# Optimization experiments

Measured on AMD Instinct MI355X. Metric: run time of the kernel, lower is better.

The kernel has to match this reference:

```python
import jax, jax.numpy as jnp
import numpy as np

N_NODES = 50000
N_EDGES = 600000
D = 128  # in_channels == out_channels
LN_EPS = 1e-5


def _mlp(h, W1, b1, W2, b2, ln_g, ln_b):
    # anemoi MLP: Linear -> SiLU -> Linear -> LayerNorm
    h = jax.nn.silu(h @ W1 + b1)
    h = h @ W2 + b2
    mu = jnp.mean(h, axis=-1, keepdims=True)
    var = jnp.var(h, axis=-1, keepdims=True)
    return (h - mu) * jax.lax.rsqrt(var + LN_EPS) * ln_g + ln_b


def setup_inputs() -> dict:
    key = jax.random.key(0)
    ks = jax.random.split(key, 12)
    s = lambda fan_in: 1.0 / np.sqrt(fan_in)
    inp = {
        "x": jax.random.normal(ks[0], (N_NODES, D), dtype=jnp.float32),
        "edge_attr": jax.random.normal(ks[1], (N_EDGES, D), dtype=jnp.float32),
        "edge_index": jax.random.randint(ks[2], (2, N_EDGES), 0, N_NODES, dtype=jnp.int32),
        # conv edge-MLP params: in = 3*D (x_dst, x_src, edge_attr)
        "eW1": jax.random.uniform(ks[3], (3 * D, D), jnp.float32, -s(3 * D), s(3 * D)),
        "eb1": jnp.zeros((D,), jnp.float32),
        "eW2": jax.random.uniform(ks[4], (D, D), jnp.float32, -s(D), s(D)),
        "eb2": jnp.zeros((D,), jnp.float32),
        "eln_g": jnp.ones((D,), jnp.float32),
        "eln_b": jnp.zeros((D,), jnp.float32),
        # node MLP params: in = 2*D (x, aggregated messages)
        "nW1": jax.random.uniform(ks[5], (2 * D, D), jnp.float32, -s(2 * D), s(2 * D)),
        "nb1": jnp.zeros((D,), jnp.float32),
        "nW2": jax.random.uniform(ks[6], (D, D), jnp.float32, -s(D), s(D)),
        "nb2": jnp.zeros((D,), jnp.float32),
        "nln_g": jnp.ones((D,), jnp.float32),
        "nln_b": jnp.zeros((D,), jnp.float32),
    }
    return inp


def reference(x, edge_attr, edge_index,
              eW1, eb1, eW2, eb2, eln_g, eln_b,
              nW1, nb1, nW2, nb2, nln_g, nln_b):
    src = edge_index[0]  # j
    dst = edge_index[1]  # i
    # GraphConv.message: edge MLP over cat([x_i, x_j, edge_attr])
    edge_in = jnp.concatenate([x[dst], x[src], edge_attr], axis=1)  # [E, 3D]
    edges_new = _mlp(edge_in, eW1, eb1, eW2, eb2, eln_g, eln_b)      # [E, D]
    # aggregate: scatter-add to destination nodes (chunking sums to the same result)
    out = jax.ops.segment_sum(edges_new, dst, num_segments=x.shape[0])  # [N, D]
    # node update: concat + MLP + residual
    nodes_new = _mlp(jnp.concatenate([x, out], axis=1), nW1, nb1, nW2, nb2, nln_g, nln_b) + x
    return nodes_new, edges_new
```

## Files before the change

kernel.cpp:

```cpp
#include <hip/hip_runtime.h>

#define D       128
#define NNODES  50000
#define NEDGES  600000
#define TE      64
#define TN      64
#define BLK     256
#define LN_EPS  1e-5f

typedef float  fx4    __attribute__((ext_vector_type(4)));
typedef float  f32x4  __attribute__((ext_vector_type(4)));
typedef __bf16 bf16x4 __attribute__((ext_vector_type(4)));
typedef __bf16 bf16x8 __attribute__((ext_vector_type(8)));

#define EW1F_OFF 0
#define EW2F_OFF (128 * 384)
#define NW1F_OFF (EW2F_OFF + 128 * 128)
#define NW2F_OFF (NW1F_OFF + 128 * 256)
#define WS_ELEMS (NW2F_OFF + 128 * 128)
#define W_BYTES  (WS_ELEMS * 2)
#define PD_OFF      ((size_t)W_BYTES)
#define PS_OFF      (PD_OFF + (size_t)NNODES * D * 4)
#define WS_NEED_PRE (PS_OFF + (size_t)NNODES * D * 4)

__device__ __forceinline__ float silu_f(float z) {
    return z * (1.0f / (1.0f + __expf(-z)));
}

__global__ __launch_bounds__(256) void prep_weights(
    const float* __restrict__ eW1, const float* __restrict__ eW2,
    const float* __restrict__ nW1, const float* __restrict__ nW2,
    __bf16* __restrict__ ws)
{
    int idx = blockIdx.x * 256 + threadIdx.x;
    if (idx >= WS_ELEMS) return;
    const float* src;
    int local;
    if (idx < EW2F_OFF)      { src = eW1; local = idx; }
    else if (idx < NW1F_OFF) { src = eW2; local = idx - EW2F_OFF; }
    else if (idx < NW2F_OFF) { src = nW1; local = idx - NW1F_OFF; }
    else                     { src = nW2; local = idx - NW2F_OFF; }
    const int f   = local >> 9;
    const int rem = local & 511;
    const int l   = rem >> 3;
    const int j   = rem & 7;
    const int ks  = f >> 3;
    const int nf  = f & 7;
    const int n   = (nf << 4) + (l & 15);
    const int k   = (ks << 5) + ((l >> 4) << 3) + j;
    ws[idx] = (__bf16)src[(size_t)k * D + n];
}

__global__ __launch_bounds__(256) void pre_nodes(
    const float* __restrict__ x,
    const __bf16* __restrict__ W1f,
    const float* __restrict__ b1,
    float* __restrict__ Pd,
    float* __restrict__ Ps)
{
    __shared__ __bf16 xt[TN][136];

    const int tid = threadIdx.x;
    const int r0g = blockIdx.x * TN;
    const int lane  = tid & 63;
    const int wid   = tid >> 6;
    const int wrow0 = wid << 4;
    const int c16   = lane & 15;
    const int kq    = lane >> 4;
    const int ks8   = kq << 3;
    const int lo8   = lane << 3;

    #pragma unroll
    for (int pass = 0; pass < 8; ++pass) {
        const int row = wrow0 + (pass << 1) + (lane >> 5);
        const int gr  = r0g + row;
        const int c4  = (lane & 31) << 2;
        fx4 v = {0.f, 0.f, 0.f, 0.f};
        if (gr < NNODES) v = *(const fx4*)&x[(size_t)gr * D + c4];
        bf16x4 h;
        #pragma unroll
        for (int j = 0; j < 4; ++j) h[j] = (__bf16)v[j];
        *(bf16x4*)&xt[row][c4] = h;
    }

    f32x4 acc_d[8], acc_s[8];
    #pragma unroll
    for (int nf = 0; nf < 8; ++nf) {
        acc_d[nf] = (f32x4){0.f, 0.f, 0.f, 0.f};
        acc_s[nf] = (f32x4){0.f, 0.f, 0.f, 0.f};
    }

    #pragma unroll
    for (int ks = 0; ks < 4; ++ks) {
        bf16x8 a = *(const bf16x8*)&xt[wrow0 + c16][(ks << 5) + ks8];
        const __bf16* wpd = W1f + ((size_t)(ks << 3) << 9) + lo8;
        const __bf16* wps = W1f + ((size_t)((4 + ks) << 3) << 9) + lo8;
        #pragma unroll
        for (int nf = 0; nf < 8; ++nf) {
            bf16x8 bd = *(const bf16x8*)(wpd + (nf << 9));
            bf16x8 bs = *(const bf16x8*)(wps + (nf << 9));
            acc_d[nf] = __builtin_amdgcn_mfma_f32_16x16x32_bf16(a, bd, acc_d[nf], 0, 0, 0);
            acc_s[nf] = __builtin_amdgcn_mfma_f32_16x16x32_bf16(a, bs, acc_s[nf], 0, 0, 0);
        }
    }

    #pragma unroll
    for (int nf = 0; nf < 8; ++nf) {
        const int col = nf * 16 + c16;
        const float bb = b1[col];
        #pragma unroll
        for (int r = 0; r < 4; ++r) {
            const int row = r0g + wrow0 + kq * 4 + r;
            if (row < NNODES) {
                Pd[(size_t)row * D + col] = acc_d[nf][r] + bb;
                Ps[(size_t)row * D + col] = acc_s[nf][r];
            }
        }
    }
}

__global__ __launch_bounds__(BLK, 5) void edge_kernel_pre(
    const float* __restrict__ edge_attr,
    const int*   __restrict__ edge_index,
    const float* __restrict__ Pd,
    const float* __restrict__ Ps,
    const __bf16* __restrict__ W1f,
    const __bf16* __restrict__ W2f,
    const float* __restrict__ b2,
    const float* __restrict__ lng, const float* __restrict__ lnb,
    float* __restrict__ edges_out,
    float* __restrict__ agg)
{
    __shared__ __bf16 sum_t[TE][136];

    const int tid = threadIdx.x;
    const int e0g = blockIdx.x * TE;
    const int lane  = tid & 63;
    const int wid   = tid >> 6;
    const int wrow0 = wid << 4;
    const int c16   = lane & 15;
    const int kq    = lane >> 4;
    const int ks8   = kq << 3;
    const int lo8   = lane << 3;

    #pragma unroll
    for (int pass = 0; pass < 8; ++pass) {
        const int row = wrow0 + (pass << 1) + (lane >> 5);
        const int ge  = e0g + row;
        const int dn  = edge_index[NEDGES + ge];
        const int sn  = edge_index[ge];
        const int c4  = (lane & 31) << 2;
        fx4 a = *(const fx4*)&Pd[(size_t)dn * D + c4];
        fx4 b = *(const fx4*)&Ps[(size_t)sn * D + c4];
        bf16x4 h;
        #pragma unroll
        for (int j = 0; j < 4; ++j) h[j] = (__bf16)(a[j] + b[j]);
        *(bf16x4*)&sum_t[row][c4] = h;
    }

    bf16x8 aE[4];
    {
        const float* ep = edge_attr + (size_t)(e0g + wrow0 + c16) * D + ks8;
        #pragma unroll
        for (int ks2 = 0; ks2 < 4; ++ks2) {
            fx4 v0 = *(const fx4*)(ep + (ks2 << 5));
            fx4 v1 = *(const fx4*)(ep + (ks2 << 5) + 4);
            bf16x8 a;
            #pragma unroll
            for (int j = 0; j < 4; ++j) { a[j] = (__bf16)v0[j]; a[j + 4] = (__bf16)v1[j]; }
            aE[ks2] = a;
        }
    }

    f32x4 acc[8];
    #pragma unroll
    for (int nf = 0; nf < 8; ++nf) acc[nf] = (f32x4){0.f, 0.f, 0.f, 0.f};

    #pragma unroll
    for (int ks2 = 0; ks2 < 4; ++ks2) {
        const __bf16* wp = W1f + ((size_t)((8 + ks2) << 3) << 9) + lo8;
        #pragma unroll
        for (int nf = 0; nf < 8; ++nf) {
            bf16x8 b = *(const bf16x8*)(wp + (nf << 9));
            acc[nf] = __builtin_amdgcn_mfma_f32_16x16x32_bf16(aE[ks2], b, acc[nf], 0, 0, 0);
        }
    }

    #pragma unroll
    for (int nf = 0; nf < 8; ++nf) {
        #pragma unroll
        for (int r = 0; r < 4; ++r) {
            const int row = wrow0 + kq * 4 + r;
            const int col = nf * 16 + c16;
            float z = acc[nf][r] + (float)sum_t[row][col];
            sum_t[row][col] = (__bf16)silu_f(z);
        }
    }

    f32x4 acc2[8];
    #pragma unroll
    for (int nf = 0; nf < 8; ++nf) acc2[nf] = (f32x4){0.f, 0.f, 0.f, 0.f};

    #pragma unroll
    for (int ks = 0; ks < 4; ++ks) {
        bf16x8 a = *(const bf16x8*)&sum_t[wrow0 + c16][(ks << 5) + ks8];
        const __bf16* wp = W2f + ((size_t)(ks << 3) << 9) + lo8;
        #pragma unroll
        for (int nf = 0; nf < 8; ++nf) {
            bf16x8 b = *(const bf16x8*)(wp + (nf << 9));
            acc2[nf] = __builtin_amdgcn_mfma_f32_16x16x32_bf16(a, b, acc2[nf], 0, 0, 0);
        }
    }

    float b2v[8], gv[8], bvv[8];
    #pragma unroll
    for (int nf = 0; nf < 8; ++nf) {
        b2v[nf] = b2[nf * 16 + c16];
        gv[nf]  = lng[nf * 16 + c16];
        bvv[nf] = lnb[nf * 16 + c16];
    }

    float s[4] = {0.f, 0.f, 0.f, 0.f}, q[4] = {0.f, 0.f, 0.f, 0.f};
    #pragma unroll
    for (int nf = 0; nf < 8; ++nf)
        #pragma unroll
        for (int r = 0; r < 4; ++r) {
            float zz = acc2[nf][r] + b2v[nf];
            acc2[nf][r] = zz;
            s[r] += zz;
            q[r] += zz * zz;
        }
    #pragma unroll
    for (int m = 1; m <= 8; m <<= 1)
        #pragma unroll
        for (int r = 0; r < 4; ++r) {
            s[r] += __shfl_xor(s[r], m, 64);
            q[r] += __shfl_xor(q[r], m, 64);
        }

    #pragma unroll
    for (int r = 0; r < 4; ++r) {
        const float mu   = s[r] * (1.0f / 128.0f);
        const float var  = q[r] * (1.0f / 128.0f) - mu * mu;
        const float rstd = rsqrtf(var + LN_EPS);
        const int row = wrow0 + kq * 4 + r;
        const int ge  = e0g + row;
        const int dn  = edge_index[NEDGES + ge];
        const size_t erow = (size_t)ge * D;
        float* ap = agg + (size_t)dn * D;
        #pragma unroll
        for (int nf = 0; nf < 8; ++nf) {
            const int col = nf * 16 + c16;
            float o = (acc2[nf][r] - mu) * rstd * gv[nf] + bvv[nf];
            edges_out[erow + col] = o;
            atomicAdd(ap + col, o);
        }
    }
}

__global__ __launch_bounds__(BLK, 4) void edge_kernel_fb(
    const float* __restrict__ x,
    const float* __restrict__ edge_attr,
    const int*   __restrict__ edge_index,
    const __bf16* __restrict__ W1f,
    const float* __restrict__ b1,
    const __bf16* __restrict__ W2f,
    const float* __restrict__ b2,
    const float* __restrict__ lng, const float* __restrict__ lnb,
    float* __restrict__ edges_out,
    float* __restrict__ agg)
{
    __shared__ __bf16 in_t[TE][264];
    __shared__ int    src_s[TE], dst_s[TE];

    const int tid = threadIdx.x;
    const int e0g = blockIdx.x * TE;

    if (tid < TE) {
        src_s[tid] = edge_index[e0g + tid];
        dst_s[tid] = edge_index[NEDGES + e0g + tid];
    }
    __syncthreads();

    const int lane  = tid & 63;
    const int wid   = tid >> 6;
    const int wrow0 = wid << 4;
    const int c16   = lane & 15;
    const int kq    = lane >> 4;
    const int ks8   = kq << 3;
    const int lo8   = lane << 3;

    bf16x8 aE[4];
    {
        const float* ep = edge_attr + (size_t)(e0g + wrow0 + c16) * D + ks8;
        #pragma unroll
        for (int ks2 = 0; ks2 < 4; ++ks2) {
            fx4 v0 = *(const fx4*)(ep + (ks2 << 5));
            fx4 v1 = *(const fx4*)(ep + (ks2 << 5) + 4);
            bf16x8 a;
            #pragma unroll
            for (int j = 0; j < 4; ++j) { a[j] = (__bf16)v0[j]; a[j + 4] = (__bf16)v1[j]; }
            aE[ks2] = a;
        }
    }

    #pragma unroll
    for (int it = 0; it < 8; ++it) {
        const int idx = tid + it * BLK;
        const int e   = idx >> 5;
        const int c4  = (idx & 31) << 2;
        fx4 v = *(const fx4*)&x[(size_t)dst_s[e] * D + c4];
        bf16x4 h;
        #pragma unroll
        for (int j = 0; j < 4; ++j) h[j] = (__bf16)v[j];
        *(bf16x4*)&in_t[e][c4] = h;
    }
    #pragma unroll
    for (int it = 0; it < 8; ++it) {
        const int idx = tid + it * BLK;
        const int e   = idx >> 5;
        const int c4  = (idx & 31) << 2;
        fx4 v = *(const fx4*)&x[(size_t)src_s[e] * D + c4];
        bf16x4 h;
        #pragma unroll
        for (int j = 0; j < 4; ++j) h[j] = (__bf16)v[j];
        *(bf16x4*)&in_t[e][128 + c4] = h;
    }
    __syncthreads();

    f32x4 acc[8];
    #pragma unroll
    for (int nf = 0; nf < 8; ++nf) acc[nf] = (f32x4){0.f, 0.f, 0.f, 0.f};

    #pragma unroll
    for (int ks = 0; ks < 12; ++ks) {
        bf16x8 a = (ks < 8) ? *(const bf16x8*)&in_t[wrow0 + c16][(ks << 5) + ks8]
                            : aE[ks - 8];
        const __bf16* wp = W1f + ((size_t)(ks << 3) << 9) + lo8;
        #pragma unroll
        for (int nf = 0; nf < 8; ++nf) {
            bf16x8 b = *(const bf16x8*)(wp + (nf << 9));
            acc[nf] = __builtin_amdgcn_mfma_f32_16x16x32_bf16(a, b, acc[nf], 0, 0, 0);
        }
    }

    #pragma unroll
    for (int nf = 0; nf < 8; ++nf) {
        const float bb = b1[nf * 16 + c16];
        #pragma unroll
        for (int r = 0; r < 4; ++r) {
            float h = silu_f(acc[nf][r] + bb);
            in_t[wrow0 + kq * 4 + r][nf * 16 + c16] = (__bf16)h;
        }
    }

    f32x4 acc2[8];
    #pragma unroll
    for (int nf = 0; nf < 8; ++nf) acc2[nf] = (f32x4){0.f, 0.f, 0.f, 0.f};

    #pragma unroll
    for (int ks = 0; ks < 4; ++ks) {
        bf16x8 a = *(const bf16x8*)&in_t[wrow0 + c16][(ks << 5) + ks8];
        const __bf16* wp = W2f + ((size_t)(ks << 3) << 9) + lo8;
        #pragma unroll
        for (int nf = 0; nf < 8; ++nf) {
            bf16x8 b = *(const bf16x8*)(wp + (nf << 9));
            acc2[nf] = __builtin_amdgcn_mfma_f32_16x16x32_bf16(a, b, acc2[nf], 0, 0, 0);
        }
    }

    float b2v[8], gv[8], bvv[8];
    #pragma unroll
    for (int nf = 0; nf < 8; ++nf) {
        b2v[nf] = b2[nf * 16 + c16];
        gv[nf]  = lng[nf * 16 + c16];
        bvv[nf] = lnb[nf * 16 + c16];
    }

    float s[4] = {0.f, 0.f, 0.f, 0.f}, q[4] = {0.f, 0.f, 0.f, 0.f};
    #pragma unroll
    for (int nf = 0; nf < 8; ++nf)
        #pragma unroll
        for (int r = 0; r < 4; ++r) {
            float zz = acc2[nf][r] + b2v[nf];
            acc2[nf][r] = zz;
            s[r] += zz;
            q[r] += zz * zz;
        }
    #pragma unroll
    for (int m = 1; m <= 8; m <<= 1)
        #pragma unroll
        for (int r = 0; r < 4; ++r) {
            s[r] += __shfl_xor(s[r], m, 64);
            q[r] += __shfl_xor(q[r], m, 64);
        }

    #pragma unroll
    for (int r = 0; r < 4; ++r) {
        const float mu   = s[r] * (1.0f / 128.0f);
        const float var  = q[r] * (1.0f / 128.0f) - mu * mu;
        const float rstd = rsqrtf(var + LN_EPS);
        const int row = wrow0 + kq * 4 + r;
        const size_t erow = (size_t)(e0g + row) * D;
        float* ap = agg + (size_t)dst_s[row] * D;
        #pragma unroll
        for (int nf = 0; nf < 8; ++nf) {
            const int col = nf * 16 + c16;
            float o = (acc2[nf][r] - mu) * rstd * gv[nf] + bvv[nf];
            edges_out[erow + col] = o;
            atomicAdd(ap + col, o);
        }
    }
}

__global__ __launch_bounds__(BLK, 4) void node_kernel(
    const float* __restrict__ x,
    const float* __restrict__ agg,
    const __bf16* __restrict__ W1f,
    const float* __restrict__ b1,
    const __bf16* __restrict__ W2f,
    const float* __restrict__ b2,
    const float* __restrict__ lng, const float* __restrict__ lnb,
    float* __restrict__ nodes_out)
{
    __shared__ __bf16 in_t[TN][264];

    const int tid = threadIdx.x;
    const int r0g = blockIdx.x * TN;

    #pragma unroll
    for (int it = 0; it < 8; ++it) {
        const int idx = tid + it * BLK;
        const int e   = idx >> 5;
        const int c4  = (idx & 31) << 2;
        const int row = r0g + e;
        fx4 v = {0.f, 0.f, 0.f, 0.f};
        if (row < NNODES) v = *(const fx4*)&x[(size_t)row * D + c4];
        bf16x4 h;
        #pragma unroll
        for (int j = 0; j < 4; ++j) h[j] = (__bf16)v[j];
        *(bf16x4*)&in_t[e][c4] = h;
    }
    #pragma unroll
    for (int it = 0; it < 8; ++it) {
        const int idx = tid + it * BLK;
        const int e   = idx >> 5;
        const int c4  = (idx & 31) << 2;
        const int row = r0g + e;
        fx4 v = {0.f, 0.f, 0.f, 0.f};
        if (row < NNODES) v = *(const fx4*)&agg[(size_t)row * D + c4];
        bf16x4 h;
        #pragma unroll
        for (int j = 0; j < 4; ++j) h[j] = (__bf16)v[j];
        *(bf16x4*)&in_t[e][128 + c4] = h;
    }
    __syncthreads();

    const int lane  = tid & 63;
    const int wid   = tid >> 6;
    const int wrow0 = wid << 4;
    const int c16   = lane & 15;
    const int kq    = lane >> 4;
    const int ks8   = kq << 3;
    const int lo8   = lane << 3;

    f32x4 acc[8];
    #pragma unroll
    for (int nf = 0; nf < 8; ++nf) acc[nf] = (f32x4){0.f, 0.f, 0.f, 0.f};

    #pragma unroll
    for (int ks = 0; ks < 8; ++ks) {
        bf16x8 a = *(const bf16x8*)&in_t[wrow0 + c16][(ks << 5) + ks8];
        const __bf16* wp = W1f + ((size_t)(ks << 3) << 9) + lo8;
        #pragma unroll
        for (int nf = 0; nf < 8; ++nf) {
            bf16x8 b = *(const bf16x8*)(wp + (nf << 9));
            acc[nf] = __builtin_amdgcn_mfma_f32_16x16x32_bf16(a, b, acc[nf], 0, 0, 0);
        }
    }

    #pragma unroll
    for (int nf = 0; nf < 8; ++nf) {
        const float bb = b1[nf * 16 + c16];
        #pragma unroll
        for (int r = 0; r < 4; ++r) {
            float h = silu_f(acc[nf][r] + bb);
            in_t[wrow0 + kq * 4 + r][nf * 16 + c16] = (__bf16)h;
        }
    }

    f32x4 acc2[8];
    #pragma unroll
    for (int nf = 0; nf < 8; ++nf) acc2[nf] = (f32x4){0.f, 0.f, 0.f, 0.f};

    #pragma unroll
    for (int ks = 0; ks < 4; ++ks) {
        bf16x8 a = *(const bf16x8*)&in_t[wrow0 + c16][(ks << 5) + ks8];
        const __bf16* wp = W2f + ((size_t)(ks << 3) << 9) + lo8;
        #pragma unroll
        for (int nf = 0; nf < 8; ++nf) {
            bf16x8 b = *(const bf16x8*)(wp + (nf << 9));
            acc2[nf] = __builtin_amdgcn_mfma_f32_16x16x32_bf16(a, b, acc2[nf], 0, 0, 0);
        }
    }

    float b2v[8], gv[8], bvv[8];
    #pragma unroll
    for (int nf = 0; nf < 8; ++nf) {
        b2v[nf] = b2[nf * 16 + c16];
        gv[nf]  = lng[nf * 16 + c16];
        bvv[nf] = lnb[nf * 16 + c16];
    }

    float s[4] = {0.f, 0.f, 0.f, 0.f}, q[4] = {0.f, 0.f, 0.f, 0.f};
    #pragma unroll
    for (int nf = 0; nf < 8; ++nf)
        #pragma unroll
        for (int r = 0; r < 4; ++r) {
            float zz = acc2[nf][r] + b2v[nf];
            acc2[nf][r] = zz;
            s[r] += zz;
            q[r] += zz * zz;
        }
    #pragma unroll
    for (int m = 1; m <= 8; m <<= 1)
        #pragma unroll
        for (int r = 0; r < 4; ++r) {
            s[r] += __shfl_xor(s[r], m, 64);
            q[r] += __shfl_xor(q[r], m, 64);
        }

    #pragma unroll
    for (int r = 0; r < 4; ++r) {
        const float mu   = s[r] * (1.0f / 128.0f);
        const float var  = q[r] * (1.0f / 128.0f) - mu * mu;
        const float rstd = rsqrtf(var + LN_EPS);
        const int row = r0g + wrow0 + kq * 4 + r;
        if (row >= NNODES) continue;
        const size_t orow = (size_t)row * D;
        #pragma unroll
        for (int nf = 0; nf < 8; ++nf) {
            const int col = nf * 16 + c16;
            float o = (acc2[nf][r] - mu) * rstd * gv[nf] + bvv[nf] + x[orow + col];
            nodes_out[orow + col] = o;
        }
    }
}

extern "C" void kernel_launch(void* const* d_in, const int* in_sizes, int n_in,
                              void* d_out, int out_size, void* d_ws, size_t ws_size,
                              hipStream_t stream) {
    (void)in_sizes; (void)n_in; (void)out_size;

    const float* x         = (const float*)d_in[0];
    const float* edge_attr = (const float*)d_in[1];
    const int*   edge_idx  = (const int*)  d_in[2];
    const float* eW1 = (const float*)d_in[3];
    const float* eb1 = (const float*)d_in[4];
    const float* eW2 = (const float*)d_in[5];
    const float* eb2 = (const float*)d_in[6];
    const float* elg = (const float*)d_in[7];
    const float* elb = (const float*)d_in[8];
    const float* nW1 = (const float*)d_in[9];
    const float* nb1 = (const float*)d_in[10];
    const float* nW2 = (const float*)d_in[11];
    const float* nb2 = (const float*)d_in[12];
    const float* nlg = (const float*)d_in[13];
    const float* nlb = (const float*)d_in[14];

    float* out       = (float*)d_out;
    float* nodes_out = out;
    float* edges_out = out + (size_t)NNODES * D;

    char*   wsb = (char*)d_ws;
    __bf16* ws  = (__bf16*)d_ws;

    prep_weights<<<(WS_ELEMS + 255) / 256, 256, 0, stream>>>(eW1, eW2, nW1, nW2, ws);

    hipMemsetAsync(nodes_out, 0, (size_t)NNODES * D * sizeof(float), stream);

    if (ws_size >= WS_NEED_PRE) {
        float* Pd = (float*)(wsb + PD_OFF);
        float* Ps = (float*)(wsb + PS_OFF);

        pre_nodes<<<(NNODES + TN - 1) / TN, BLK, 0, stream>>>(
            x, ws + EW1F_OFF, eb1, Pd, Ps);

        edge_kernel_pre<<<NEDGES / TE, BLK, 0, stream>>>(
            edge_attr, edge_idx, Pd, Ps,
            ws + EW1F_OFF, ws + EW2F_OFF, eb2, elg, elb,
            edges_out, nodes_out);
    } else {
        edge_kernel_fb<<<NEDGES / TE, BLK, 0, stream>>>(
            x, edge_attr, edge_idx,
            ws + EW1F_OFF, eb1, ws + EW2F_OFF, eb2, elg, elb,
            edges_out, nodes_out);
    }

    node_kernel<<<(NNODES + TN - 1) / TN, BLK, 0, stream>>>(
        x, nodes_out,
        ws + NW1F_OFF, nb1, ws + NW2F_OFF, nb2, nlg, nlb,
        nodes_out);
}
```

Measured before the change: 520.9 us.

## Sort edges by destination into CSR and aggregate in shared memory

Builds a destination-sorted edge list on the device (histogram, single-block scan, scatter), then launches one edge block per 64 destination nodes. Each block accumulates its messages in a shared-memory fp32 tile and writes it once, which replaces global atomics and the memset of the output. The per-node projections Pd/Ps are also stored in bf16 to halve gather traffic. Risks: four extra small launches, including a serial one-block scan, load imbalance across node blocks with different degrees, lower occupancy from the larger shared tile, and edge_attr/edges_out accessed in permuted order.

```diff
diff --git a/kernel.cpp b/kernel.cpp
--- a/kernel.cpp
+++ b/kernel.cpp
@@ -19,9 +19,13 @@
 #define NW2F_OFF (NW1F_OFF + 128 * 256)
 #define WS_ELEMS (NW2F_OFF + 128 * 128)
 #define W_BYTES  (WS_ELEMS * 2)
-#define PD_OFF      ((size_t)W_BYTES)
-#define PS_OFF      (PD_OFF + (size_t)NNODES * D * 4)
-#define WS_NEED_PRE (PS_OFF + (size_t)NNODES * D * 4)
+#define PDB_OFF     ((size_t)W_BYTES)
+#define PSB_OFF     (PDB_OFF + (size_t)NNODES * D * 2)
+#define COUNTS_OFF  (PSB_OFF + (size_t)NNODES * D * 2)
+#define OFFS_OFF    (COUNTS_OFF + 4 * (size_t)NNODES)
+#define CURS_OFF    (OFFS_OFF   + 4 * ((size_t)NNODES + 1))
+#define ELIST_OFF   (CURS_OFF   + 4 * (size_t)NNODES)
+#define WS_NEED     (ELIST_OFF  + 4 * (size_t)NEDGES)
 
 __device__ __forceinline__ float silu_f(float z) {
     return z * (1.0f / (1.0f + __expf(-z)));
@@ -51,12 +55,63 @@
     ws[idx] = (__bf16)src[(size_t)k * D + n];
 }
 
+__global__ __launch_bounds__(256) void hist_kernel(
+    const int* __restrict__ edge_index, int* __restrict__ counts)
+{
+    int i = blockIdx.x * 256 + threadIdx.x;
+    if (i < NEDGES) atomicAdd(&counts[edge_index[NEDGES + i]], 1);
+}
+
+__global__ __launch_bounds__(256) void scan_kernel(
+    const int* __restrict__ counts, int* __restrict__ offs, int* __restrict__ curs)
+{
+    __shared__ int sh[256];
+    const int t = threadIdx.x;
+    const int STRIP = (NNODES + 255) / 256;
+    const int base = t * STRIP;
+
+    int tsum = 0;
+    for (int i = 0; i < STRIP; ++i) {
+        int idx = base + i;
+        if (idx < NNODES) tsum += counts[idx];
+    }
+    sh[t] = tsum;
+    __syncthreads();
+    for (int off = 1; off < 256; off <<= 1) {
+        int add = (t >= off) ? sh[t - off] : 0;
+        __syncthreads();
+        sh[t] += add;
+        __syncthreads();
+    }
+    int run = (t > 0) ? sh[t - 1] : 0;
+    for (int i = 0; i < STRIP; ++i) {
+        int idx = base + i;
+        if (idx < NNODES) {
+            offs[idx] = run;
+            curs[idx] = run;
+            run += counts[idx];
+        }
+    }
+    if (t == 255) offs[NNODES] = run;
+}
+
+__global__ __launch_bounds__(256) void scatter_kernel(
+    const int* __restrict__ edge_index, int* __restrict__ curs,
+    int* __restrict__ elist)
+{
+    int i = blockIdx.x * 256 + threadIdx.x;
+    if (i < NEDGES) {
+        int pos = atomicAdd(&curs[edge_index[NEDGES + i]], 1);
+        elist[pos] = i;
+    }
+}
+
 __global__ __launch_bounds__(256) void pre_nodes(
     const float* __restrict__ x,
     const __bf16* __restrict__ W1f,
     const float* __restrict__ b1,
-    float* __restrict__ Pd,
-    float* __restrict__ Ps)
+    __bf16* __restrict__ PdB,
+    __bf16* __restrict__ PsB)
 {
     __shared__ __bf16 xt[TN][136];
 
@@ -112,29 +167,38 @@
         for (int r = 0; r < 4; ++r) {
             const int row = r0g + wrow0 + kq * 4 + r;
             if (row < NNODES) {
-                Pd[(size_t)row * D + col] = acc_d[nf][r] + bb;
-                Ps[(size_t)row * D + col] = acc_s[nf][r];
-            }
-        }
-    }
-}
-
-__global__ __launch_bounds__(BLK, 5) void edge_kernel_pre(
+                PdB[(size_t)row * D + col] = (__bf16)(acc_d[nf][r] + bb);
+                PsB[(size_t)row * D + col] = (__bf16)acc_s[nf][r];
+            }
+        }
+    }
+}
+
+__global__ __launch_bounds__(BLK, 3) void edge_kernel_csr(
     const float* __restrict__ edge_attr,
     const int*   __restrict__ edge_index,
-    const float* __restrict__ Pd,
-    const float* __restrict__ Ps,
+    const __bf16* __restrict__ PdB,
+    const __bf16* __restrict__ PsB,
     const __bf16* __restrict__ W1f,
     const __bf16* __restrict__ W2f,
     const float* __restrict__ b2,
     const float* __restrict__ lng, const float* __restrict__ lnb,
+    const int*   __restrict__ offs,
+    const int*   __restrict__ elist,
     float* __restrict__ edges_out,
     float* __restrict__ agg)
 {
-    __shared__ __bf16 sum_t[TE][136];
+    __shared__ float  aggF[64][132];
+    __shared__ __bf16 sum_t[64][136];
+    __shared__ int    ce[64], cd[64], cs[64];
 
     const int tid = threadIdx.x;
-    const int e0g = blockIdx.x * TE;
+    const int n0  = blockIdx.x * 64;
+
+    #pragma unroll
+    for (int i = tid; i < 64 * 132; i += BLK) ((float*)aggF)[i] = 0.f;
+    __syncthreads();
+
     const int lane  = tid & 63;
     const int wid   = tid >> 6;
     const int wrow0 = wid << 4;
@@ -143,74 +207,9 @@
     const int ks8   = kq << 3;
     const int lo8   = lane << 3;
 
-    #pragma unroll
-    for (int pass = 0; pass < 8; ++pass) {
-        const int row = wrow0 + (pass << 1) + (lane >> 5);
-        const int ge  = e0g + row;
-        const int dn  = edge_index[NEDGES + ge];
-        const int sn  = edge_index[ge];
-        const int c4  = (lane & 31) << 2;
-        fx4 a = *(const fx4*)&Pd[(size_t)dn * D + c4];
-        fx4 b = *(const fx4*)&Ps[(size_t)sn * D + c4];
-        bf16x4 h;
-        #pragma unroll
-        for (int j = 0; j < 4; ++j) h[j] = (__bf16)(a[j] + b[j]);
-        *(bf16x4*)&sum_t[row][c4] = h;
-    }
-
-    bf16x8 aE[4];
-    {
-        const float* ep = edge_attr + (size_t)(e0g + wrow0 + c16) * D + ks8;
-        #pragma unroll
-        for (int ks2 = 0; ks2 < 4; ++ks2) {
-            fx4 v0 = *(const fx4*)(ep + (ks2 << 5));
-            fx4 v1 = *(const fx4*)(ep + (ks2 << 5) + 4);
-            bf16x8 a;
-            #pragma unroll
-            for (int j = 0; j < 4; ++j) { a[j] = (__bf16)v0[j]; a[j + 4] = (__bf16)v1[j]; }
-            aE[ks2] = a;
-        }
-    }
-
-    f32x4 acc[8];
-    #pragma unroll
-    for (int nf = 0; nf < 8; ++nf) acc[nf] = (f32x4){0.f, 0.f, 0.f, 0.f};
-
-    #pragma unroll
-    for (int ks2 = 0; ks2 < 4; ++ks2) {
-        const __bf16* wp = W1f + ((size_t)((8 + ks2) << 3) << 9) + lo8;
-        #pragma unroll
-        for (int nf = 0; nf < 8; ++nf) {
-            bf16x8 b = *(const bf16x8*)(wp + (nf << 9));
-            acc[nf] = __builtin_amdgcn_mfma_f32_16x16x32_bf16(aE[ks2], b, acc[nf], 0, 0, 0);
-        }
-    }
-
-    #pragma unroll
-    for (int nf = 0; nf < 8; ++nf) {
-        #pragma unroll
-        for (int r = 0; r < 4; ++r) {
-            const int row = wrow0 + kq * 4 + r;
-            const int col = nf * 16 + c16;
-            float z = acc[nf][r] + (float)sum_t[row][col];
-            sum_t[row][col] = (__bf16)silu_f(z);
-        }
-    }
-
-    f32x4 acc2[8];
-    #pragma unroll
-    for (int nf = 0; nf < 8; ++nf) acc2[nf] = (f32x4){0.f, 0.f, 0.f, 0.f};
-
-    #pragma unroll
-    for (int ks = 0; ks < 4; ++ks) {
-        bf16x8 a = *(const bf16x8*)&sum_t[wrow0 + c16][(ks << 5) + ks8];
-        const __bf16* wp = W2f + ((size_t)(ks << 3) << 9) + lo8;
-        #pragma unroll
-        for (int nf = 0; nf < 8; ++nf) {
-            bf16x8 b = *(const bf16x8*)(wp + (nf << 9));
-            acc2[nf] = __builtin_amdgcn_mfma_f32_16x16x32_bf16(a, b, acc2[nf], 0, 0, 0);
-        }
-    }
+    const int nHi  = (n0 + 64 < NNODES) ? n0 + 64 : NNODES;
+    const int eBeg = offs[n0];
+    const int eEnd = offs[nHi];
 
     float b2v[8], gv[8], bvv[8];
     #pragma unroll
@@ -220,41 +219,129 @@
         bvv[nf] = lnb[nf * 16 + c16];
     }
 
-    float s[4] = {0.f, 0.f, 0.f, 0.f}, q[4] = {0.f, 0.f, 0.f, 0.f};
-    #pragma unroll
-    for (int nf = 0; nf < 8; ++nf)
-        #pragma unroll
-        for (int r = 0; r < 4; ++r) {
-            float zz = acc2[nf][r] + b2v[nf];
-            acc2[nf][r] = zz;
-            s[r] += zz;
-            q[r] += zz * zz;
-        }
-    #pragma unroll
-    for (int m = 1; m <= 8; m <<= 1)
-        #pragma unroll
-        for (int r = 0; r < 4; ++r) {
-            s[r] += __shfl_xor(s[r], m, 64);
-            q[r] += __shfl_xor(q[r], m, 64);
-        }
-
-    #pragma unroll
-    for (int r = 0; r < 4; ++r) {
-        const float mu   = s[r] * (1.0f / 128.0f);
-        const float var  = q[r] * (1.0f / 128.0f) - mu * mu;
-        const float rstd = rsqrtf(var + LN_EPS);
-        const int row = wrow0 + kq * 4 + r;
-        const int ge  = e0g + row;
-        const int dn  = edge_index[NEDGES + ge];
-        const size_t erow = (size_t)ge * D;
-        float* ap = agg + (size_t)dn * D;
-        #pragma unroll
-        for (int nf = 0; nf < 8; ++nf) {
-            const int col = nf * 16 + c16;
-            float o = (acc2[nf][r] - mu) * rstd * gv[nf] + bvv[nf];
-            edges_out[erow + col] = o;
-            atomicAdd(ap + col, o);
-        }
+    for (int c = eBeg; c < eEnd; c += 64) {
+        if (lane < 16) {
+            const int row = wrow0 + lane;
+            int p = c + row;
+            if (p >= eEnd) p = eEnd - 1;
+            const int eid = elist[p];
+            ce[row] = eid;
+            cd[row] = edge_index[NEDGES + eid];
+            cs[row] = edge_index[eid];
+        }
+
+        #pragma unroll
+        for (int pass = 0; pass < 8; ++pass) {
+            const int row = wrow0 + (pass << 1) + (lane >> 5);
+            const int dn = cd[row], sn = cs[row];
+            const int c4 = (lane & 31) << 2;
+            bf16x4 a = *(const bf16x4*)&PdB[(size_t)dn * D + c4];
+            bf16x4 b = *(const bf16x4*)&PsB[(size_t)sn * D + c4];
+            bf16x4 h;
+            #pragma unroll
+            for (int j = 0; j < 4; ++j) h[j] = (__bf16)((float)a[j] + (float)b[j]);
+            *(bf16x4*)&sum_t[row][c4] = h;
+        }
+
+        bf16x8 aE[4];
+        {
+            const float* ep = edge_attr + (size_t)ce[wrow0 + c16] * D + ks8;
+            #pragma unroll
+            for (int ks2 = 0; ks2 < 4; ++ks2) {
+                fx4 v0 = *(const fx4*)(ep + (ks2 << 5));
+                fx4 v1 = *(const fx4*)(ep + (ks2 << 5) + 4);
+                bf16x8 a;
+                #pragma unroll
+                for (int j = 0; j < 4; ++j) { a[j] = (__bf16)v0[j]; a[j + 4] = (__bf16)v1[j]; }
+                aE[ks2] = a;
+            }
+        }
+
+        f32x4 acc[8];
+        #pragma unroll
+        for (int nf = 0; nf < 8; ++nf) acc[nf] = (f32x4){0.f, 0.f, 0.f, 0.f};
+
+        #pragma unroll
+        for (int ks2 = 0; ks2 < 4; ++ks2) {
+            const __bf16* wp = W1f + ((size_t)((8 + ks2) << 3) << 9) + lo8;
+            #pragma unroll
+            for (int nf = 0; nf < 8; ++nf) {
+                bf16x8 b = *(const bf16x8*)(wp + (nf << 9));
+                acc[nf] = __builtin_amdgcn_mfma_f32_16x16x32_bf16(aE[ks2], b, acc[nf], 0, 0, 0);
+            }
+        }
+
+        #pragma unroll
+        for (int nf = 0; nf < 8; ++nf) {
+            #pragma unroll
+            for (int r = 0; r < 4; ++r) {
+                const int row = wrow0 + kq * 4 + r;
+                const int col = nf * 16 + c16;
+                float z = acc[nf][r] + (float)sum_t[row][col];
+                sum_t[row][col] = (__bf16)silu_f(z);
+            }
+        }
+
+        f32x4 acc2[8];
+        #pragma unroll
+        for (int nf = 0; nf < 8; ++nf) acc2[nf] = (f32x4){0.f, 0.f, 0.f, 0.f};
+
+        #pragma unroll
+        for (int ks = 0; ks < 4; ++ks) {
+            bf16x8 a = *(const bf16x8*)&sum_t[wrow0 + c16][(ks << 5) + ks8];
+            const __bf16* wp = W2f + ((size_t)(ks << 3) << 9) + lo8;
+            #pragma unroll
+            for (int nf = 0; nf < 8; ++nf) {
+                bf16x8 b = *(const bf16x8*)(wp + (nf << 9));
+                acc2[nf] = __builtin_amdgcn_mfma_f32_16x16x32_bf16(a, b, acc2[nf], 0, 0, 0);
+            }
+        }
+
+        float s[4] = {0.f, 0.f, 0.f, 0.f}, q[4] = {0.f, 0.f, 0.f, 0.f};
+        #pragma unroll
+        for (int nf = 0; nf < 8; ++nf)
+            #pragma unroll
+            for (int r = 0; r < 4; ++r) {
+                float zz = acc2[nf][r] + b2v[nf];
+                acc2[nf][r] = zz;
+                s[r] += zz;
+                q[r] += zz * zz;
+            }
+        #pragma unroll
+        for (int m = 1; m <= 8; m <<= 1)
+            #pragma unroll
+            for (int r = 0; r < 4; ++r) {
+                s[r] += __shfl_xor(s[r], m, 64);
+                q[r] += __shfl_xor(q[r], m, 64);
+            }
+
+        #pragma unroll
+        for (int r = 0; r < 4; ++r) {
+            const int row = wrow0 + kq * 4 + r;
+            if (c + row < eEnd) {
+                const float mu   = s[r] * (1.0f / 128.0f);
+                const float var  = q[r] * (1.0f / 128.0f) - mu * mu;
+                const float rstd = rsqrtf(var + LN_EPS);
+                const int eid = ce[row];
+                const int dl  = cd[row] - n0;
+                const size_t erow = (size_t)eid * D;
+                #pragma unroll
+                for (int nf = 0; nf < 8; ++nf) {
+                    const int col = nf * 16 + c16;
+                    float o = (acc2[nf][r] - mu) * rstd * gv[nf] + bvv[nf];
+                    edges_out[erow + col] = o;
+                    atomicAdd(&aggF[dl][col], o);
+                }
+            }
+        }
+    }
+
+    __syncthreads();
+    #pragma unroll
+    for (int i = tid; i < 64 * 128; i += BLK) {
+        const int row = i >> 7, col = i & 127;
+        const int g = n0 + row;
+        if (g < NNODES) agg[(size_t)g * D + col] = aggF[row][col];
     }
 }
 
@@ -577,20 +664,28 @@
 
     prep_weights<<<(WS_ELEMS + 255) / 256, 256, 0, stream>>>(eW1, eW2, nW1, nW2, ws);
 
-    hipMemsetAsync(nodes_out, 0, (size_t)NNODES * D * sizeof(float), stream);
-
-    if (ws_size >= WS_NEED_PRE) {
-        float* Pd = (float*)(wsb + PD_OFF);
-        float* Ps = (float*)(wsb + PS_OFF);
+    if (ws_size >= WS_NEED) {
+        __bf16* PdB  = (__bf16*)(wsb + PDB_OFF);
+        __bf16* PsB  = (__bf16*)(wsb + PSB_OFF);
+        int* counts  = (int*)(wsb + COUNTS_OFF);
+        int* offs    = (int*)(wsb + OFFS_OFF);
+        int* curs    = (int*)(wsb + CURS_OFF);
+        int* elist   = (int*)(wsb + ELIST_OFF);
 
         pre_nodes<<<(NNODES + TN - 1) / TN, BLK, 0, stream>>>(
-            x, ws + EW1F_OFF, eb1, Pd, Ps);
-
-        edge_kernel_pre<<<NEDGES / TE, BLK, 0, stream>>>(
-            edge_attr, edge_idx, Pd, Ps,
+            x, ws + EW1F_OFF, eb1, PdB, PsB);
+
+        hipMemsetAsync(counts, 0, NNODES * sizeof(int), stream);
+        hist_kernel<<<(NEDGES + 255) / 256, 256, 0, stream>>>(edge_idx, counts);
+        scan_kernel<<<1, 256, 0, stream>>>(counts, offs, curs);
+        scatter_kernel<<<(NEDGES + 255) / 256, 256, 0, stream>>>(edge_idx, curs, elist);
+
+        edge_kernel_csr<<<(NNODES + 63) / 64, BLK, 0, stream>>>(
+            edge_attr, edge_idx, PdB, PsB,
             ws + EW1F_OFF, ws + EW2F_OFF, eb2, elg, elb,
-            edges_out, nodes_out);
+            offs, elist, edges_out, nodes_out);
     } else {
+        hipMemsetAsync(nodes_out, 0, (size_t)NNODES * D * sizeof(float), stream);
         edge_kernel_fb<<<NEDGES / TE, BLK, 0, stream>>>(
             x, edge_attr, edge_idx,
             ws + EW1F_OFF, eb1, ws + EW2F_OFF, eb2, elg, elb,
```

Result: slower. 1.339 ms (+157.0%).
